# Kernel optimization log

Hardware: AMD Instinct MI355X
Metric: run time of the kernel (lower is better)

## Reference

```python
import jax, jax.numpy as jnp
import numpy as np

N = 100000   # nodes
E = 1600000  # edges
IN_DIM, HID, HEADS, OUT_DIM = 8, 64, 4, 3


def _add_self_loops(src, dst, n):
    loop = jnp.arange(n, dtype=src.dtype)
    return jnp.concatenate([src, loop]), jnp.concatenate([dst, loop])


def gcn_conv(x, src, dst, n, W, b):
    # PyG GCNConv: add self-loops, symmetric normalization deg^-1/2 * deg^-1/2
    s, d = _add_self_loops(src, dst, n)
    deg = jax.ops.segment_sum(jnp.ones(s.shape[0], x.dtype), d, num_segments=n)
    dinv = jnp.where(deg > 0, jax.lax.rsqrt(deg), 0.0)
    norm = dinv[s] * dinv[d]                       # [E']
    h = x @ W                                      # [N, out]
    out = jax.ops.segment_sum(norm[:, None] * h[s], d, num_segments=n)
    return out + b


def gat_conv(x, src, dst, n, W, att_src, att_dst, b):
    # PyG GATConv, concat=True, negative_slope=0.2, self-loops added
    h = (x @ W).reshape(n, HEADS, HID)             # [N, H, C]
    s, d = _add_self_loops(src, dst, n)
    a_src = jnp.sum(h * att_src, axis=-1)          # [N, H]
    a_dst = jnp.sum(h * att_dst, axis=-1)          # [N, H]
    e = jax.nn.leaky_relu(a_src[s] + a_dst[d], negative_slope=0.2)  # [E', H]
    m = jax.lax.stop_gradient(jax.ops.segment_max(e, d, num_segments=n))
    ex = jnp.exp(e - m[d])
    denom = jax.ops.segment_sum(ex, d, num_segments=n)
    alpha = ex / (denom[d] + 1e-16)                # segment softmax over incoming edges
    out = jax.ops.segment_sum(alpha[:, :, None] * h[s], d, num_segments=n)  # [N, H, C]
    return out.reshape(n, HEADS * HID) + b


def setup_inputs() -> dict:
    key = jax.random.key(0)
    ks = jax.random.split(key, 16)
    def glorot(k, shape):
        fan = shape[0] + shape[-1]
        return jax.random.normal(k, shape, jnp.float32) * np.sqrt(2.0 / fan)
    return {
        "x": jax.random.normal(ks[0], (N, IN_DIM), jnp.float32),
        "edge_index": jax.random.randint(ks[1], (2, E), 0, N, jnp.int64 if jax.config.jax_enable_x64 else jnp.int32),
        "w1": glorot(ks[2], (IN_DIM, HID)), "b1": jnp.zeros((HID,), jnp.float32),
        "w2": glorot(ks[3], (HID, HID)),   "b2": jnp.zeros((HID,), jnp.float32),
        "w3": glorot(ks[4], (HID, HID)),   "b3": jnp.zeros((HID,), jnp.float32),
        "wg": glorot(ks[5], (HID, HEADS * HID)), "bg": jnp.zeros((HEADS * HID,), jnp.float32),
        "att_src": glorot(ks[6], (HEADS, HID)),
        "att_dst": glorot(ks[7], (HEADS, HID)),
        "wc1": glorot(ks[8], (HEADS * HID, HID)), "bc1": jnp.zeros((HID,), jnp.float32),
        "wc2": glorot(ks[9], (HID, OUT_DIM)),     "bc2": jnp.zeros((OUT_DIM,), jnp.float32),
    }


def reference(x, edge_index, w1, b1, w2, b2, w3, b3, wg, bg, att_src, att_dst, wc1, bc1, wc2, bc2):
    src, dst = edge_index[0], edge_index[1]
    n = x.shape[0]
    # stacked GCN convs with ReLU; residual when shapes match (layers 2,3)
    h = jax.nn.relu(gcn_conv(x, src, dst, n, w1, b1))
    h = h + jax.nn.relu(gcn_conv(h, src, dst, n, w2, b2))
    h = h + jax.nn.relu(gcn_conv(h, src, dst, n, w3, b3))
    # GAT attention layer (4 heads, concat)
    h_att = gat_conv(h, src, dst, n, wg, att_src, att_dst, bg)  # [N, 256]
    # classifier MLP (dropout is inference no-op)
    z = jax.nn.relu(h_att @ wc1 + bc1)
    logits = z @ wc2 + bc2
    return jax.nn.log_softmax(logits, axis=1)
```

## Files before the change

kernel.cpp:

```cpp
#include <hip/hip_runtime.h>
#include <math.h>


typedef _Float16 half8 __attribute__((ext_vector_type(8)));
typedef _Float16 f16x8 __attribute__((ext_vector_type(8)));
typedef float f32x4 __attribute__((ext_vector_type(4)));
typedef int int4v __attribute__((ext_vector_type(4)));

#define BCAP 210000

__device__ __forceinline__ float leaky02(float v) { return v > 0.f ? v : 0.2f * v; }


template <int CTRL>
__device__ __forceinline__ float dpp_add(float v) {
    int iv = __builtin_bit_cast(int, v);
    int r = __builtin_amdgcn_update_dpp(iv, iv, CTRL, 0xF, 0xF, false);
    return v + __builtin_bit_cast(float, r);
}
template <int OFF>
__device__ __forceinline__ float swz_add(float v) {
    int r = __builtin_amdgcn_ds_swizzle(__builtin_bit_cast(int, v), OFF);
    return v + __builtin_bit_cast(float, r);
}
template <int CTRL>
__device__ __forceinline__ float dpp_max(float v) {
    int iv = __builtin_bit_cast(int, v);
    int r = __builtin_amdgcn_update_dpp(iv, iv, CTRL, 0xF, 0xF, false);
    return fmaxf(v, __builtin_bit_cast(float, r));
}
template <int OFF>
__device__ __forceinline__ float swz_max(float v) {
    int r = __builtin_amdgcn_ds_swizzle(__builtin_bit_cast(int, v), OFF);
    return fmaxf(v, __builtin_bit_cast(float, r));
}
__device__ __forceinline__ float red8(float v) {
    v = dpp_add<0xB1>(v);
    v = dpp_add<0x4E>(v);
    v = swz_add<0x101F>(v);
    return v;
}
__device__ __forceinline__ float red16(float v) {
    v = dpp_add<0xB1>(v);
    v = dpp_add<0x4E>(v);
    v = swz_add<0x101F>(v);
    v = dpp_add<0x128>(v);
    return v;
}
__device__ __forceinline__ float red16max(float v) {
    v = dpp_max<0xB1>(v);
    v = dpp_max<0x4E>(v);
    v = swz_max<0x101F>(v);
    v = dpp_max<0x128>(v);
    return v;
}
__device__ __forceinline__ float red64(float v) {
    v = dpp_add<0xB1>(v);
    v = dpp_add<0x4E>(v);
    v = swz_add<0x101F>(v);
    v = dpp_add<0x128>(v);
    v = swz_add<0x401F>(v);
    v = v + __shfl_xor(v, 32);
    return v;
}
__device__ __forceinline__ float red32max(float v) {
    v = dpp_max<0xB1>(v);
    v = dpp_max<0x4E>(v);
    v = swz_max<0x101F>(v);
    v = dpp_max<0x128>(v);
    v = swz_max<0x401F>(v);
    return v;
}


__global__ __launch_bounds__(256) void bucketize(
        const int* __restrict__ src, const int* __restrict__ dst,
        int E, int range,
        int* __restrict__ bucketCur, int* __restrict__ bSrc, int* __restrict__ bDst) {
    __shared__ unsigned sScan[4][256];
    __shared__ unsigned long long sPair[2048];
    __shared__ int sBase[8];
    __shared__ int sLds[9];
    int tid = threadIdx.x;
    int e0 = blockIdx.x * 2048 + tid * 8;

    int d[8], s[8], rr[8];
    bool ok[8];
    if (e0 + 7 < E) {
        int4v da = *(const int4v*)(dst + e0);
        int4v db = *(const int4v*)(dst + e0 + 4);
        int4v sa = *(const int4v*)(src + e0);
        int4v sb = *(const int4v*)(src + e0 + 4);
#pragma unroll
        for (int j = 0; j < 4; ++j) { d[j] = da[j]; d[j + 4] = db[j]; s[j] = sa[j]; s[j + 4] = sb[j]; ok[j] = true; ok[j + 4] = true; }
    } else {
#pragma unroll
        for (int j = 0; j < 8; ++j) {
            ok[j] = (e0 + j < E);
            d[j] = ok[j] ? dst[e0 + j] : 0;
            s[j] = ok[j] ? src[e0 + j] : 0;
        }
    }
    unsigned hcnt = 0;
#pragma unroll
    for (int j = 0; j < 8; ++j) {
        int r = min(d[j] / range, 7);
        rr[j] = r;
        if (ok[j]) hcnt += 1u << (r * 4);
    }
#pragma unroll
    for (int k = 0; k < 4; ++k)
        sScan[k][tid] = ((hcnt >> (k * 8)) & 0xF) | (((hcnt >> (k * 8 + 4)) & 0xF) << 16);
    __syncthreads();
    for (int off = 1; off < 256; off <<= 1) {
        unsigned v0 = (tid >= off) ? sScan[0][tid - off] : 0;
        unsigned v1 = (tid >= off) ? sScan[1][tid - off] : 0;
        unsigned v2 = (tid >= off) ? sScan[2][tid - off] : 0;
        unsigned v3 = (tid >= off) ? sScan[3][tid - off] : 0;
        __syncthreads();
        sScan[0][tid] += v0; sScan[1][tid] += v1; sScan[2][tid] += v2; sScan[3][tid] += v3;
        __syncthreads();
    }
    if (tid < 8) {
        int k = tid >> 1, sh = (tid & 1) * 16;
        int tot = (sScan[k][255] >> sh) & 0xFFFF;
        sBase[tid] = atomicAdd(&bucketCur[tid], tot);
    }
    if (tid == 0) {
        int run = 0;
#pragma unroll
        for (int r = 0; r < 8; ++r) {
            sLds[r] = run;
            run += (sScan[r >> 1][255] >> ((r & 1) * 16)) & 0xFFFF;
        }
        sLds[8] = run;
    }
    __syncthreads();
    unsigned placed = 0;
#pragma unroll
    for (int j = 0; j < 8; ++j) {
        if (ok[j]) {
            int r = rr[j];
            int k = r >> 1, sh = (r & 1) * 16;
            int incl = (sScan[k][tid] >> sh) & 0xFFFF;
            int mine = (hcnt >> (r * 4)) & 0xF;
            int ex = incl - mine;
            int pc = (placed >> (r * 4)) & 0xF;
            placed += 1u << (r * 4);
            sPair[sLds[r] + ex + pc] =
                ((unsigned long long)(unsigned)d[j] << 32) | (unsigned)s[j];
        }
    }
    __syncthreads();
    int btotal = sLds[8];
    for (int i = tid; i < btotal; i += 256) {
        unsigned long long p = sPair[i];
        int r = 0;
#pragma unroll
        for (int k = 1; k < 8; ++k) r += (i >= sLds[k]);
        size_t g = (size_t)r * BCAP + sBase[r] + (i - sLds[r]);
        bSrc[g] = (int)(unsigned)(p & 0xFFFFFFFFu);
        bDst[g] = (int)(unsigned)(p >> 32);
    }
}

__global__ void count_b(const int* __restrict__ bDst,
                        const int* __restrict__ bucketCur,
                        int* __restrict__ counts) {
    int grp = blockIdx.x & 7;
    int cnt = bucketCur[grp];
    const int* bd = bDst + (size_t)grp * BCAP;
    int nblk = gridDim.x >> 3;
    int c = blockIdx.x >> 3;
    int stride4 = nblk * blockDim.x * 4;
    for (int e = (c * blockDim.x + threadIdx.x) * 4; e < cnt; e += stride4) {
        if (e + 3 < cnt) {
            int4v d4 = *(const int4v*)(bd + e);
#pragma unroll
            for (int j = 0; j < 4; ++j) atomicAdd(&counts[d4[j]], 1);
        } else {
#pragma unroll
            for (int j = 0; j < 4; ++j)
                if (e + j < cnt) atomicAdd(&counts[bd[e + j]], 1);
        }
    }
}

__global__ void scan_pass1(const int* __restrict__ counts, int n, int* __restrict__ blockSums) {
    __shared__ int sh[256];
    int base = blockIdx.x * 2048;
    int tid = threadIdx.x;
    int s = 0;
#pragma unroll
    for (int j = 0; j < 8; ++j) {
        int idx = base + tid * 8 + j;
        if (idx < n) s += counts[idx];
    }
    sh[tid] = s;
    __syncthreads();
    for (int off = 128; off > 0; off >>= 1) {
        if (tid < off) sh[tid] += sh[tid + off];
        __syncthreads();
    }
    if (tid == 0) blockSums[blockIdx.x] = sh[0];
}

__global__ void scan_pass2(const int* __restrict__ blockSums, int nb, int* __restrict__ blockOffs) {
    if (threadIdx.x == 0 && blockIdx.x == 0) {
        int run = 0;
        for (int i = 0; i < nb; ++i) { blockOffs[i] = run; run += blockSums[i]; }
    }
}

__global__ void scan_pass3(const int* __restrict__ counts, int n,
                           const int* __restrict__ blockOffs,
                           const float* __restrict__ x,
                           int* __restrict__ row_ptr, int* __restrict__ cursor,
                           float* __restrict__ dinv, float* __restrict__ rdinv,
                           _Float16* __restrict__ xs,
                           int* __restrict__ shortList, int* __restrict__ longList,
                           int* __restrict__ nodeCnts) {
    __shared__ int sh[256];
    __shared__ int shp[256];
    __shared__ int baseS, baseL;
    int base = blockIdx.x * 2048;
    int tid = threadIdx.x;
    int cnt[8];
    int local = 0;
#pragma unroll
    for (int j = 0; j < 8; ++j) {
        int idx = base + tid * 8 + j;
        cnt[j] = (idx < n) ? counts[idx] : 0;
        local += cnt[j];
    }
    sh[tid] = local;
    __syncthreads();
    for (int off = 1; off < 256; off <<= 1) {
        int v = (tid >= off) ? sh[tid - off] : 0;
        __syncthreads();
        sh[tid] += v;
        __syncthreads();
    }
    int run = blockOffs[blockIdx.x] + sh[tid] - local;
#pragma unroll
    for (int j = 0; j < 8; ++j) {
        int idx = base + tid * 8 + j;
        if (idx < n) {
            row_ptr[idx] = run;
            cursor[idx] = run;
            float dv = rsqrtf((float)(cnt[j] + 1));
            dinv[idx] = dv;
            rdinv[idx] = sqrtf((float)(cnt[j] + 1));
#pragma unroll
            for (int t = 0; t < 8; ++t) xs[idx * 8 + t] = (_Float16)(dv * x[idx * 8 + t]);
            run += cnt[j];
            if (idx == n - 1) row_ptr[n] = run;
        }
    }
    int myS = 0, myL = 0;
#pragma unroll
    for (int j = 0; j < 8; ++j) {
        int idx = base + tid * 8 + j;
        if (idx < n) { if (cnt[j] <= 15) ++myS; else ++myL; }
    }
    shp[tid] = myS | (myL << 16);
    __syncthreads();
    for (int off = 1; off < 256; off <<= 1) {
        int v = (tid >= off) ? shp[tid - off] : 0;
        __syncthreads();
        shp[tid] += v;
        __syncthreads();
    }
    if (tid == 255) {
        baseS = atomicAdd(&nodeCnts[0], shp[255] & 0xFFFF);
        baseL = atomicAdd(&nodeCnts[1], shp[255] >> 16);
    }
    __syncthreads();
    int pS = baseS + (shp[tid] & 0xFFFF) - myS;
    int pL = baseL + (shp[tid] >> 16) - myL;
#pragma unroll
    for (int j = 0; j < 8; ++j) {
        int idx = base + tid * 8 + j;
        if (idx < n) {
            if (cnt[j] <= 15) shortList[pS++] = idx;
            else              longList[pL++] = idx;
        }
    }
}

__global__ void scatter_b(const int* __restrict__ bSrc, const int* __restrict__ bDst,
                          const int* __restrict__ bucketCur,
                          int* __restrict__ cursor, int* __restrict__ col_src) {
    int grp = blockIdx.x & 7;
    int cnt = bucketCur[grp];
    const int* bd = bDst + (size_t)grp * BCAP;
    const int* bs = bSrc + (size_t)grp * BCAP;
    int nblk = gridDim.x >> 3;
    int c = blockIdx.x >> 3;
    int stride4 = nblk * blockDim.x * 4;
    for (int e = (c * blockDim.x + threadIdx.x) * 4; e < cnt; e += stride4) {
        if (e + 3 < cnt) {
            int4v d4 = *(const int4v*)(bd + e);
            int4v s4 = *(const int4v*)(bs + e);
#pragma unroll
            for (int j = 0; j < 4; ++j) {
                int pos = atomicAdd(&cursor[d4[j]], 1);
                col_src[pos] = s4[j];
            }
        } else {
#pragma unroll
            for (int j = 0; j < 4; ++j) {
                if (e + j < cnt) {
                    int pos = atomicAdd(&cursor[bd[e + j]], 1);
                    col_src[pos] = bs[e + j];
                }
            }
        }
    }
}


__global__ void ccomb_kernel(const float* __restrict__ Wg, const float* __restrict__ bg,
                             const float* __restrict__ wc1, const float* __restrict__ bc1,
                             const float* __restrict__ att_src, const float* __restrict__ att_dst,
                             const float* __restrict__ w2, const float* __restrict__ w3,
                             _Float16* __restrict__ CcombP, float* __restrict__ bcomb,
                             float* __restrict__ wse, float* __restrict__ wde,
                             _Float16* __restrict__ W2P, _Float16* __restrict__ W3P) {
    int bid = blockIdx.x;
    int j = threadIdx.x;
    if (bid < 256) {
        int i = bid;
        float s = 0.f;
        for (int c = 0; c < 64; ++c)
            s += Wg[(i & 63) * 256 + (i >> 6) * 64 + c] * wc1[((i >> 6) * 64 + c) * 64 + j];
        _Float16 hi = (_Float16)s;
        _Float16 lo = (_Float16)(s - (float)hi);
        int kt = i >> 5, l = (((i >> 3) & 3) << 4) | (j & 15), e = i & 7, ct = j >> 4;
        CcombP[(ct * 8 + kt) * 512 + l * 8 + e] = hi;
        CcombP[(32 + ct * 8 + kt) * 512 + l * 8 + e] = lo;
    } else if (bid == 256) {
        float s = bc1[j];
        for (int i = 0; i < 256; ++i) s += bg[i] * wc1[i * 64 + j];
        bcomb[j] = s;
#pragma unroll
        for (int h = 0; h < 4; ++h) {
            float ss = 0.f, sd = 0.f;
            for (int c = 0; c < 64; ++c) {
                float w = Wg[j * 256 + h * 64 + c];
                ss += w * att_src[h * 64 + c];
                sd += w * att_dst[h * 64 + c];
            }
            wse[j * 4 + h] = ss;
            wde[j * 4 + h] = sd;
        }
    } else {
        int i = (bid < 321) ? (bid - 257) : (bid - 321);
        const float* W = (bid < 321) ? w2 : w3;
        _Float16* WP = (bid < 321) ? W2P : W3P;
        float s = W[i * 64 + j];
        _Float16 hi = (_Float16)s;
        _Float16 lo = (_Float16)(s - (float)hi);
        int kt = i >> 5, l = (((i >> 3) & 3) << 4) | (j & 15), e = i & 7, ct = j >> 4;
        WP[(ct * 2 + kt) * 512 + l * 8 + e] = hi;
        WP[(8 + ct * 2 + kt) * 512 + l * 8 + e] = lo;
    }
}


__global__ void gcn_layer1(const half8* __restrict__ xs8,
                           const float* __restrict__ W1, const float* __restrict__ b1,
                           const int* __restrict__ row_ptr, const int* __restrict__ col_src,
                           const float* __restrict__ dinv, int n,
                           _Float16* __restrict__ hs1) {
    int tid = threadIdx.x, lane = tid & 63, wid = tid >> 6;
    int node = blockIdx.x * 4 + wid;
    if (node >= n) return;
    int beg = row_ptr[node], end = row_ptr[node + 1];
    int deg = end - beg;
    float acc[8] = {0.f, 0.f, 0.f, 0.f, 0.f, 0.f, 0.f, 0.f};
    for (int base = 0; base < deg; base += 64) {
        int cs = col_src[min(beg + base + lane, end - 1)];
        half8 v = xs8[cs];
        if (base + lane < deg) {
#pragma unroll
            for (int c = 0; c < 8; ++c) acc[c] += (float)v[c];
        }
    }
#pragma unroll
    for (int c = 0; c < 8; ++c) acc[c] = red64(acc[c]);
    half8 sv = xs8[node];
    float di = dinv[node];
    float agg[8];
#pragma unroll
    for (int c = 0; c < 8; ++c) agg[c] = (acc[c] + (float)sv[c]) * di;
    float sum = b1[lane];
#pragma unroll
    for (int k = 0; k < 8; ++k) sum = fmaf(agg[k], W1[k * 64 + lane], sum);
    hs1[node * 64 + lane] = (_Float16)(di * fmaxf(sum, 0.f));
}


__global__ void gcn_agg(const _Float16* __restrict__ hs_in,
                        const int* __restrict__ row_ptr, const int* __restrict__ col_src,
                        const float* __restrict__ dinv, int n,
                        _Float16* __restrict__ aggout) {
    int tid = threadIdx.x, lane = tid & 63, wid = tid >> 6;
    int node = blockIdx.x * 4 + wid;
    if (node >= n) return;
    int t = lane >> 3, g = lane & 7;
    const half8* hs8 = (const half8*)hs_in;
    int beg = row_ptr[node], end = row_ptr[node + 1];
    int deg = end - beg;
    half8 sv = hs8[node * 8 + t];
    float ac[8];
#pragma unroll
    for (int c = 0; c < 8; ++c) ac[c] = (g == 0) ? (float)sv[c] : 0.f;
    for (int base = 0; base < deg; base += 64) {
        int cs = col_src[min(beg + base + lane, end - 1)];
        int lim = min(deg - base, 64);
        auto bodyF = [&](int eo8) {
            int s = __shfl(cs, eo8 + g);
            half8 v = hs8[s * 8 + t];
#pragma unroll
            for (int c = 0; c < 8; ++c) ac[c] += (float)v[c];
        };
        auto bodyG = [&](int eo8) {
            int eo = eo8 + g;
            int s = __shfl(cs, eo);
            half8 v = hs8[s * 8 + t];
            if (eo < lim) {
#pragma unroll
                for (int c = 0; c < 8; ++c) ac[c] += (float)v[c];
            }
        };
        int eo8 = 0;
        for (; eo8 + 16 <= lim; eo8 += 16) { bodyF(eo8); bodyF(eo8 + 8); }
        if (eo8 < lim) {
            bodyG(eo8);
            eo8 += 8;
            if (eo8 < lim) bodyG(eo8);
        }
    }
    float di = dinv[node];
#pragma unroll
    for (int c = 0; c < 8; ++c) ac[c] = red8(ac[c]) * di;
    if (g == 0) {
        half8 hv;
#pragma unroll
        for (int c = 0; c < 8; ++c) hv[c] = (_Float16)ac[c];
        *(half8*)(aggout + (size_t)node * 64 + t * 8) = hv;
    }
}


template <bool LAST>
__global__ __launch_bounds__(256) void gcn_mfma(
        const _Float16* __restrict__ agg,
        const _Float16* __restrict__ WP,
        const float* __restrict__ b,
        const _Float16* __restrict__ hs_in,
        const float* __restrict__ dinv, const float* __restrict__ rdinv,
        const float* __restrict__ wse, const float* __restrict__ wde,
        int n, _Float16* __restrict__ hout,
        float4* __restrict__ a_src4, float4* __restrict__ a_dst4) {
    __shared__ float partS[4][16][4];
    __shared__ float partD[4][16][4];
    int tid = threadIdx.x;
    int lane = tid & 63;
    int w = __builtin_amdgcn_readfirstlane(tid >> 6);
    int c16 = lane & 15, hi = lane >> 4;

    f16x8 bh[2], blo[2];
#pragma unroll
    for (int kt = 0; kt < 2; ++kt) {
        bh[kt]  = *(const f16x8*)(WP + (size_t)(w * 2 + kt) * 512 + lane * 8);
        blo[kt] = *(const f16x8*)(WP + (size_t)(8 + w * 2 + kt) * 512 + lane * 8);
    }
    int col = w * 16 + c16;
    float bl = b[col];
    float4 wev, wdv;
    if (LAST) {
        wev = ((const float4*)wse)[col];
        wdv = ((const float4*)wde)[col];
    }

    int ntiles = (n + 15) >> 4;
    for (int tile = blockIdx.x; tile < ntiles; tile += gridDim.x) {
        int rowb = tile * 16;
        int arow = min(rowb + c16, n - 1);
        const _Float16* ap = agg + (size_t)arow * 64 + hi * 8;
        f16x8 a0 = *(const f16x8*)(ap);
        f16x8 a1 = *(const f16x8*)(ap + 32);
        f32x4 acc = {0.f, 0.f, 0.f, 0.f};
        acc = __builtin_amdgcn_mfma_f32_16x16x32_f16(a0, bh[0],  acc, 0, 0, 0);
        acc = __builtin_amdgcn_mfma_f32_16x16x32_f16(a0, blo[0], acc, 0, 0, 0);
        acc = __builtin_amdgcn_mfma_f32_16x16x32_f16(a1, bh[1],  acc, 0, 0, 0);
        acc = __builtin_amdgcn_mfma_f32_16x16x32_f16(a1, blo[1], acc, 0, 0, 0);
#pragma unroll
        for (int r = 0; r < 4; ++r) {
            int noder = rowb + hi * 4 + r;
            bool ok = noder < n;
            int ni = min(noder, n - 1);
            float hp = rdinv[ni] * (float)hs_in[(size_t)ni * 64 + col];
            float z = fmaxf(acc[r] + bl, 0.f);
            float hv = hp + z;
            if (!LAST) {
                if (ok) hout[(size_t)ni * 64 + col] = (_Float16)(dinv[ni] * hv);
            } else {
                if (ok) hout[(size_t)ni * 64 + col] = (_Float16)hv;
                float s0 = red16(hv * wev.x), s1 = red16(hv * wev.y);
                float s2 = red16(hv * wev.z), s3 = red16(hv * wev.w);
                float d0 = red16(hv * wdv.x), d1 = red16(hv * wdv.y);
                float d2 = red16(hv * wdv.z), d3 = red16(hv * wdv.w);
                if (c16 == 0) {
                    *(float4*)&partS[w][hi * 4 + r][0] = make_float4(s0, s1, s2, s3);
                    *(float4*)&partD[w][hi * 4 + r][0] = make_float4(d0, d1, d2, d3);
                }
            }
        }
        if (LAST) {
            __syncthreads();
            if (tid < 16) {
                int node = rowb + tid;
                if (node < n) {
                    float4 s = make_float4(
                        partS[0][tid][0] + partS[1][tid][0] + partS[2][tid][0] + partS[3][tid][0],
                        partS[0][tid][1] + partS[1][tid][1] + partS[2][tid][1] + partS[3][tid][1],
                        partS[0][tid][2] + partS[1][tid][2] + partS[2][tid][2] + partS[3][tid][2],
                        partS[0][tid][3] + partS[1][tid][3] + partS[2][tid][3] + partS[3][tid][3]);
                    float4 d = make_float4(
                        partD[0][tid][0] + partD[1][tid][0] + partD[2][tid][0] + partD[3][tid][0],
                        partD[0][tid][1] + partD[1][tid][1] + partD[2][tid][1] + partD[3][tid][1],
                        partD[0][tid][2] + partD[1][tid][2] + partD[2][tid][2] + partD[3][tid][2],
                        partD[0][tid][3] + partD[1][tid][3] + partD[2][tid][3] + partD[3][tid][3]);
                    a_src4[node] = s;
                    a_dst4[node] = d;
                }
            }
            __syncthreads();
        }
    }
}


__global__ __launch_bounds__(256, 4) void gat_agg_short(
        const _Float16* __restrict__ h3,
        const float4* __restrict__ a_src4, const float4* __restrict__ a_dst4,
        const int* __restrict__ row_ptr, const int* __restrict__ col_src,
        const int* __restrict__ shortList, const int* __restrict__ nodeCnts,
        _Float16* __restrict__ aggout) {
    __shared__ _Float16 HsAll[4][32 * 72];
    __shared__ _Float16 wATAll[4][16 * 40];
    int tid = threadIdx.x, lane = tid & 63, wid = tid >> 6;
    int nshort = nodeCnts[0];
    int i0 = (blockIdx.x * 4 + wid) * 2;
    if (i0 >= nshort) return;
    int nodeA = shortList[i0];
    int nodeB = (i0 + 1 < nshort) ? shortList[i0 + 1] : nodeA;
    _Float16* Hs = HsAll[wid];
    _Float16* wAT = wATAll[wid];

    {
        int zm = lane >> 2;
        int zc = ((zm < 8) ? 16 : 0) + (lane & 3) * 4;
#pragma unroll
        for (int j = 0; j < 4; ++j) wAT[zm * 40 + zc + j] = (_Float16)0.f;
    }

    int q = lane >> 4, m16 = lane & 15;
    int c0 = (lane & 7) * 8;
    int sl16 = lane & 15;
    int myNode = (lane < 16) ? nodeA : ((lane < 32) ? nodeB : nodeA);
    int begL = row_ptr[myNode], endL = row_ptr[myNode + 1];
    int nslL = endL - begL + 1;
    float4 adv = a_dst4[myNode];
    int eidx = max(min(begL + sl16 - 1, endL - 1), 0);
    int cs = (sl16 == 0) ? myNode : col_src[eidx];
    float4 as = a_src4[cs];
    float vm = (sl16 < nslL && lane < 32) ? 1.f : 0.f;
    float l0 = leaky02(as.x + adv.x);
    float l1 = leaky02(as.y + adv.y);
    float l2 = leaky02(as.z + adv.z);
    float l3 = leaky02(as.w + adv.w);
    float m0 = red16max(vm > 0.f ? l0 : -1e30f);
    float m1 = red16max(vm > 0.f ? l1 : -1e30f);
    float m2 = red16max(vm > 0.f ? l2 : -1e30f);
    float m3 = red16max(vm > 0.f ? l3 : -1e30f);
    float w0 = vm * __expf(fminf(l0 - m0, 10.f));
    float w1 = vm * __expf(fminf(l1 - m1, 10.f));
    float w2 = vm * __expf(fminf(l2 - m2, 10.f));
    float w3 = vm * __expf(fminf(l3 - m3, 10.f));
    if (lane < 32) {
        int rb = (lane < 16) ? 0 : 8;
        int k = lane;
        _Float16 h0 = (_Float16)w0, h1 = (_Float16)w1;
        _Float16 h2 = (_Float16)w2, h3v = (_Float16)w3;
        wAT[(rb + 0) * 40 + k] = h0;
        wAT[(rb + 1) * 40 + k] = h1;
        wAT[(rb + 2) * 40 + k] = h2;
        wAT[(rb + 3) * 40 + k] = h3v;
        wAT[(rb + 4) * 40 + k] = (_Float16)(w0 - (float)h0);
        wAT[(rb + 5) * 40 + k] = (_Float16)(w1 - (float)h1);
        wAT[(rb + 6) * 40 + k] = (_Float16)(w2 - (float)h2);
        wAT[(rb + 7) * 40 + k] = (_Float16)(w3 - (float)h3v);
    }
#pragma unroll
    for (int i = 0; i < 4; ++i) {
        int r = i * 8 + (lane >> 3);
        int s = __shfl(cs, r);
        half8 hv = *(const half8*)(h3 + (size_t)s * 64 + c0);
        *(half8*)(Hs + r * 72 + (c0 ^ (i << 4))) = hv;
    }
    __asm__ volatile("s_waitcnt lgkmcnt(0)" ::: "memory");
    f16x8 A = *(const f16x8*)(wAT + m16 * 40 + q * 8);
    int swz = q << 4;
    const _Float16* Bb0 = Hs + (size_t)q * 8 * 72 + ((0 * 16 + m16) ^ swz);
    const _Float16* Bb1 = Hs + (size_t)q * 8 * 72 + ((1 * 16 + m16) ^ swz);
    const _Float16* Bb2 = Hs + (size_t)q * 8 * 72 + ((2 * 16 + m16) ^ swz);
    const _Float16* Bb3 = Hs + (size_t)q * 8 * 72 + ((3 * 16 + m16) ^ swz);
    f16x8 B0, B1, B2, B3;
#pragma unroll
    for (int e = 0; e < 8; ++e) {
        B0[e] = Bb0[e * 72];
        B1[e] = Bb1[e * 72];
        B2[e] = Bb2[e * 72];
        B3[e] = Bb3[e * 72];
    }
    f16x8 ONES;
#pragma unroll
    for (int e = 0; e < 8; ++e) ONES[e] = (_Float16)1.f;
    f32x4 acc0 = {0.f,0.f,0.f,0.f}, acc1 = {0.f,0.f,0.f,0.f};
    f32x4 acc2 = {0.f,0.f,0.f,0.f}, acc3 = {0.f,0.f,0.f,0.f};
    f32x4 accD = {0.f,0.f,0.f,0.f};
    acc0 = __builtin_amdgcn_mfma_f32_16x16x32_f16(A, B0, acc0, 0, 0, 0);
    acc1 = __builtin_amdgcn_mfma_f32_16x16x32_f16(A, B1, acc1, 0, 0, 0);
    acc2 = __builtin_amdgcn_mfma_f32_16x16x32_f16(A, B2, acc2, 0, 0, 0);
    acc3 = __builtin_amdgcn_mfma_f32_16x16x32_f16(A, B3, acc3, 0, 0, 0);
    accD = __builtin_amdgcn_mfma_f32_16x16x32_f16(A, ONES, accD, 0, 0, 0);

    float tot[4][4], rdv[4];
#pragma unroll
    for (int r = 0; r < 4; ++r) {
        tot[0][r] = acc0[r] + __shfl_xor(acc0[r], 16);
        tot[1][r] = acc1[r] + __shfl_xor(acc1[r], 16);
        tot[2][r] = acc2[r] + __shfl_xor(acc2[r], 16);
        tot[3][r] = acc3[r] + __shfl_xor(acc3[r], 16);
        float d = accD[r] + __shfl_xor(accD[r], 16);
        rdv[r] = 1.f / (d + 1e-16f);
    }
    int outNode = -1;
    if (lane < 16) outNode = nodeA;
    else if (lane >= 32 && lane < 48 && nodeB != nodeA) outNode = nodeB;
    if (outNode >= 0) {
        size_t ob = (size_t)outNode * 256 + (lane & 15);
#pragma unroll
        for (int r = 0; r < 4; ++r) {
#pragma unroll
            for (int ct = 0; ct < 4; ++ct)
                aggout[ob + r * 64 + ct * 16] = (_Float16)(tot[ct][r] * rdv[r]);
        }
    }
}


__global__ __launch_bounds__(256, 4) void gat_agg_long(
        const _Float16* __restrict__ h3,
        const float4* __restrict__ a_src4, const float4* __restrict__ a_dst4,
        const int* __restrict__ row_ptr, const int* __restrict__ col_src,
        const int* __restrict__ longList, const int* __restrict__ nodeCnts,
        _Float16* __restrict__ aggout) {
    __shared__ _Float16 HsAll[4][32 * 72];
    __shared__ _Float16 wATAll[4][16 * 40];
    int tid = threadIdx.x, lane = tid & 63, wid = tid >> 6;
    int nlong = nodeCnts[1];
    int li = blockIdx.x * 4 + wid;
    if (li >= nlong) return;
    int node = longList[li];
    _Float16* Hs = HsAll[wid];
    _Float16* wAT = wATAll[wid];

    int q = lane >> 4, m16 = lane & 15;
    float4 ad = a_dst4[node];
    int beg = row_ptr[node], end = row_ptr[node + 1];
    int deg = end - beg;
    int nslots = deg + 1;
    int c0 = (lane & 7) * 8;

    int swz = q << 4;
    const _Float16* Bb0 = Hs + (size_t)q * 8 * 72 + ((0 * 16 + m16) ^ swz);
    const _Float16* Bb1 = Hs + (size_t)q * 8 * 72 + ((1 * 16 + m16) ^ swz);
    const _Float16* Bb2 = Hs + (size_t)q * 8 * 72 + ((2 * 16 + m16) ^ swz);
    const _Float16* Bb3 = Hs + (size_t)q * 8 * 72 + ((3 * 16 + m16) ^ swz);
    const f16x8* Ab = (const f16x8*)(wAT + m16 * 40 + q * 8);
    f16x8 ONES;
#pragma unroll
    for (int e = 0; e < 8; ++e) ONES[e] = (_Float16)1.f;

    f32x4 acc0 = {0.f,0.f,0.f,0.f}, acc1 = {0.f,0.f,0.f,0.f};
    f32x4 acc2 = {0.f,0.f,0.f,0.f}, acc3 = {0.f,0.f,0.f,0.f};
    f32x4 accD = {0.f,0.f,0.f,0.f};
    float m0 = 0.f, m1 = 0.f, m2 = 0.f, m3 = 0.f;

    for (int base = 0; base < nslots; base += 32) {
        int sl = base + (lane & 31);
        int eidx = max(min(beg + sl - 1, end - 1), 0);
        int cs = (sl == 0) ? node : col_src[eidx];
        float4 as = a_src4[cs];
        float vm = (sl < nslots && lane < 32) ? 1.f : 0.f;
        float l0 = leaky02(as.x + ad.x);
        float l1 = leaky02(as.y + ad.y);
        float l2 = leaky02(as.z + ad.z);
        float l3 = leaky02(as.w + ad.w);
        if (base == 0) {
            m0 = red32max(vm > 0.f ? l0 : -1e30f);
            m1 = red32max(vm > 0.f ? l1 : -1e30f);
            m2 = red32max(vm > 0.f ? l2 : -1e30f);
            m3 = red32max(vm > 0.f ? l3 : -1e30f);
        }
        float w0 = vm * __expf(fminf(l0 - m0, 10.f));
        float w1 = vm * __expf(fminf(l1 - m1, 10.f));
        float w2 = vm * __expf(fminf(l2 - m2, 10.f));
        float w3 = vm * __expf(fminf(l3 - m3, 10.f));
        if (lane < 32) {
            int s32 = lane & 31;
            _Float16 h0 = (_Float16)w0, h1 = (_Float16)w1;
            _Float16 h2 = (_Float16)w2, h3v = (_Float16)w3;
            wAT[0 * 40 + s32] = h0;
            wAT[1 * 40 + s32] = h1;
            wAT[2 * 40 + s32] = h2;
            wAT[3 * 40 + s32] = h3v;
            wAT[4 * 40 + s32] = (_Float16)(w0 - (float)h0);
            wAT[5 * 40 + s32] = (_Float16)(w1 - (float)h1);
            wAT[6 * 40 + s32] = (_Float16)(w2 - (float)h2);
            wAT[7 * 40 + s32] = (_Float16)(w3 - (float)h3v);
        }
#pragma unroll
        for (int i = 0; i < 4; ++i) {
            int r = i * 8 + (lane >> 3);
            int s = __shfl(cs, r);
            half8 hv = *(const half8*)(h3 + (size_t)s * 64 + c0);
            *(half8*)(Hs + r * 72 + (c0 ^ (i << 4))) = hv;
        }
        __asm__ volatile("s_waitcnt lgkmcnt(0)" ::: "memory");
        f16x8 A = *Ab;
        f16x8 B0, B1, B2, B3;
#pragma unroll
        for (int e = 0; e < 8; ++e) {
            B0[e] = Bb0[e * 72];
            B1[e] = Bb1[e * 72];
            B2[e] = Bb2[e * 72];
            B3[e] = Bb3[e * 72];
        }
        acc0 = __builtin_amdgcn_mfma_f32_16x16x32_f16(A, B0, acc0, 0, 0, 0);
        acc1 = __builtin_amdgcn_mfma_f32_16x16x32_f16(A, B1, acc1, 0, 0, 0);
        acc2 = __builtin_amdgcn_mfma_f32_16x16x32_f16(A, B2, acc2, 0, 0, 0);
        acc3 = __builtin_amdgcn_mfma_f32_16x16x32_f16(A, B3, acc3, 0, 0, 0);
        accD = __builtin_amdgcn_mfma_f32_16x16x32_f16(A, ONES, accD, 0, 0, 0);
        __asm__ volatile("s_waitcnt lgkmcnt(0)" ::: "memory");
    }

    float tot[4][4], rdv[4];
#pragma unroll
    for (int r = 0; r < 4; ++r) {
        tot[0][r] = acc0[r] + __shfl_xor(acc0[r], 16);
        tot[1][r] = acc1[r] + __shfl_xor(acc1[r], 16);
        tot[2][r] = acc2[r] + __shfl_xor(acc2[r], 16);
        tot[3][r] = acc3[r] + __shfl_xor(acc3[r], 16);
        float d = accD[r] + __shfl_xor(accD[r], 16);
        rdv[r] = 1.f / (d + 1e-16f);
    }
    if (lane < 16) {
        size_t ob = (size_t)node * 256 + lane;
#pragma unroll
        for (int r = 0; r < 4; ++r) {
#pragma unroll
            for (int ct = 0; ct < 4; ++ct)
                aggout[ob + r * 64 + ct * 16] = (_Float16)(tot[ct][r] * rdv[r]);
        }
    }
}


__global__ __launch_bounds__(256) void mlp_mfma(
        const _Float16* __restrict__ agg,
        const _Float16* __restrict__ CP,
        const float* __restrict__ bcomb,
        const float* __restrict__ wc2, const float* __restrict__ bc2,
        int n, float* __restrict__ out) {
    __shared__ float part[4][16][3];
    int tid = threadIdx.x;
    int lane = tid & 63;
    int w = __builtin_amdgcn_readfirstlane(tid >> 6);
    int c16 = lane & 15, hi = lane >> 4;

    f16x8 bh[8], blo[8];
#pragma unroll
    for (int kt = 0; kt < 8; ++kt) {
        bh[kt]  = *(const f16x8*)(CP + (size_t)(w * 8 + kt) * 512 + lane * 8);
        blo[kt] = *(const f16x8*)(CP + (size_t)(32 + w * 8 + kt) * 512 + lane * 8);
    }
    int col = w * 16 + c16;
    float bc  = bcomb[col];
    float w20 = wc2[col * 3 + 0], w21 = wc2[col * 3 + 1], w22 = wc2[col * 3 + 2];
    float bb0 = bc2[0], bb1 = bc2[1], bb2 = bc2[2];

    int ntiles = (n + 15) >> 4;
    for (int tile = blockIdx.x; tile < ntiles; tile += gridDim.x) {
        int rowb = tile * 16;
        int row = min(rowb + c16, n - 1);
        const _Float16* ap = agg + (size_t)row * 256 + hi * 8;
        f16x8 a[8];
#pragma unroll
        for (int kt = 0; kt < 8; ++kt) a[kt] = *(const f16x8*)(ap + kt * 32);
        f32x4 acc = {0.f, 0.f, 0.f, 0.f};
#pragma unroll
        for (int kt = 0; kt < 8; ++kt) {
            acc = __builtin_amdgcn_mfma_f32_16x16x32_f16(a[kt], bh[kt],  acc, 0, 0, 0);
            acc = __builtin_amdgcn_mfma_f32_16x16x32_f16(a[kt], blo[kt], acc, 0, 0, 0);
        }
        float pr[4][3];
#pragma unroll
        for (int r = 0; r < 4; ++r) {
            float z = fmaxf(acc[r] + bc, 0.f);
            pr[r][0] = red16(z * w20);
            pr[r][1] = red16(z * w21);
            pr[r][2] = red16(z * w22);
        }
        if (c16 == 0) {
#pragma unroll
            for (int r = 0; r < 4; ++r) {
                part[w][hi * 4 + r][0] = pr[r][0];
                part[w][hi * 4 + r][1] = pr[r][1];
                part[w][hi * 4 + r][2] = pr[r][2];
            }
        }
        __syncthreads();
        if (tid < 16) {
            int node = rowb + tid;
            if (node < n) {
                float e0 = part[0][tid][0] + part[1][tid][0] + part[2][tid][0] + part[3][tid][0] + bb0;
                float e1 = part[0][tid][1] + part[1][tid][1] + part[2][tid][1] + part[3][tid][1] + bb1;
                float e2 = part[0][tid][2] + part[1][tid][2] + part[2][tid][2] + part[3][tid][2] + bb2;
                float mx = fmaxf(e0, fmaxf(e1, e2));
                float lse = mx + logf(expf(e0 - mx) + expf(e1 - mx) + expf(e2 - mx));
                out[(size_t)node * 3 + 0] = e0 - lse;
                out[(size_t)node * 3 + 1] = e1 - lse;
                out[(size_t)node * 3 + 2] = e2 - lse;
            }
        }
        __syncthreads();
    }
}


extern "C" void kernel_launch(void* const* d_in, const int* in_sizes, int n_in,
                              void* d_out, int out_size, void* d_ws, size_t ws_size,
                              hipStream_t stream) {
    const float* x       = (const float*)d_in[0];
    const int*   ei      = (const int*)d_in[1];
    const float* w1      = (const float*)d_in[2];
    const float* b1      = (const float*)d_in[3];
    const float* w2      = (const float*)d_in[4];
    const float* b2      = (const float*)d_in[5];
    const float* w3      = (const float*)d_in[6];
    const float* b3      = (const float*)d_in[7];
    const float* wg      = (const float*)d_in[8];
    const float* bg      = (const float*)d_in[9];
    const float* att_s   = (const float*)d_in[10];
    const float* att_d   = (const float*)d_in[11];
    const float* wc1     = (const float*)d_in[12];
    const float* bc1     = (const float*)d_in[13];
    const float* wc2     = (const float*)d_in[14];
    const float* bc2     = (const float*)d_in[15];
    float* out = (float*)d_out;

    const int N = in_sizes[0] / 8;
    const int E = in_sizes[1] / 2;
    const int* srcv = ei;
    const int* dstv = ei + E;

    char* ws = (char*)d_ws;
    size_t off = 0;
    auto alloc = [&](size_t bytes) -> char* {
        char* p = ws + off;
        off += (bytes + 255) & ~(size_t)255;
        return p;
    };
    int*      counts    = (int*)alloc((size_t)N * 4);
    int*      row_ptr   = (int*)alloc((size_t)(N + 1) * 4);
    int*      cursor    = (int*)alloc((size_t)N * 4);
    int*      col_src   = (int*)alloc((size_t)E * 4);
    int*      blockSums = (int*)alloc(4096 * 4);
    int*      blockOffs = (int*)alloc(4096 * 4);
    float*    dinv      = (float*)alloc((size_t)N * 4);
    float*    rdinv     = (float*)alloc((size_t)N * 4);
    _Float16* xs        = (_Float16*)alloc((size_t)N * 8 * 2);
    float*    a_src     = (float*)alloc((size_t)N * 16);
    float*    a_dst     = (float*)alloc((size_t)N * 16);
    float*    wse       = (float*)alloc(256 * 4);
    float*    wde       = (float*)alloc(256 * 4);
    _Float16* CcombP    = (_Float16*)alloc(64 * 1024);
    float*    bcomb     = (float*)alloc(64 * 4);
    _Float16* W2P       = (_Float16*)alloc(16 * 1024);
    _Float16* W3P       = (_Float16*)alloc(16 * 1024);
    int*      shortList = (int*)alloc((size_t)N * 4);
    int*      longList  = (int*)alloc((size_t)N * 4);
    int*      nodeCnts  = (int*)alloc(256);
    int*      bucketCur = (int*)alloc(256);
    _Float16* bufA      = (_Float16*)alloc((size_t)N * 64 * 2);
    _Float16* bufB      = (_Float16*)alloc((size_t)N * 64 * 2);
    _Float16* aggbuf    = (_Float16*)alloc((size_t)N * 256 * 2);
    _Float16* hs1 = bufA;
    _Float16* hs2 = bufB;
    _Float16* h3  = bufA;
    _Float16* aggA = aggbuf;
    int* bSrc = (int*)aggbuf;
    int* bDst = bSrc + (size_t)8 * BCAP;
    (void)ws_size; (void)n_in; (void)out_size;

    hipMemsetAsync(counts, 0, (size_t)N * 4, stream);
    hipMemsetAsync(nodeCnts, 0, 8, stream);
    hipMemsetAsync(bucketCur, 0, 32, stream);

    const int TPB = 256;
    int range = (N + 7) / 8;

    int gridBk = (E + 2047) / 2048;
    bucketize<<<gridBk, TPB, 0, stream>>>(srcv, dstv, E, range, bucketCur, bSrc, bDst);
    count_b<<<2048, TPB, 0, stream>>>(bDst, bucketCur, counts);

    int NB = (N + 2047) / 2048;
    scan_pass1<<<NB, TPB, 0, stream>>>(counts, N, blockSums);
    scan_pass2<<<1, 64, 0, stream>>>(blockSums, NB, blockOffs);
    scan_pass3<<<NB, TPB, 0, stream>>>(counts, N, blockOffs, x,
                                       row_ptr, cursor, dinv, rdinv, xs,
                                       shortList, longList, nodeCnts);
    scatter_b<<<2048, TPB, 0, stream>>>(bSrc, bDst, bucketCur, cursor, col_src);

    ccomb_kernel<<<385, 64, 0, stream>>>(wg, bg, wc1, bc1, att_s, att_d, w2, w3,
                                         CcombP, bcomb, wse, wde, W2P, W3P);

    int gridN = (N + 3) / 4;
    gcn_layer1<<<gridN, TPB, 0, stream>>>((const half8*)xs, w1, b1, row_ptr, col_src,
                                          dinv, N, hs1);

    gcn_agg<<<gridN, TPB, 0, stream>>>(hs1, row_ptr, col_src, dinv, N, aggA);
    gcn_mfma<false><<<2048, TPB, 0, stream>>>(aggA, W2P, b2, hs1, dinv, rdinv,
                                              nullptr, nullptr, N, hs2,
                                              nullptr, nullptr);
    gcn_agg<<<gridN, TPB, 0, stream>>>(hs2, row_ptr, col_src, dinv, N, aggA);
    gcn_mfma<true><<<2048, TPB, 0, stream>>>(aggA, W3P, b3, hs2, dinv, rdinv,
                                             wse, wde, N, h3,
                                             (float4*)a_src, (float4*)a_dst);

    int gridS = ((N + 1) / 2 + 3) / 4;
    gat_agg_short<<<gridS, TPB, 0, stream>>>(h3, (const float4*)a_src,
                                             (const float4*)a_dst, row_ptr, col_src,
                                             shortList, nodeCnts, aggbuf);
    gat_agg_long<<<gridN, TPB, 0, stream>>>(h3, (const float4*)a_src,
                                            (const float4*)a_dst, row_ptr, col_src,
                                            longList, nodeCnts, aggbuf);
    mlp_mfma<<<2048, TPB, 0, stream>>>(aggbuf, CcombP, bcomb, wc2, bc2, N, out);
}
```

Baseline: 530.0 us.

## Assign edge buckets to blocks by XCC id with atomic work-stealing tickets

Measured after the change: 871.9 us. 1.65x slower.

```diff
diff --git a/kernel.cpp b/kernel.cpp
--- a/kernel.cpp
+++ b/kernel.cpp
@@ -10,6 +10,12 @@
 #define BCAP 210000
 
 __device__ __forceinline__ float leaky02(float v) { return v > 0.f ? v : 0.2f * v; }
+
+__device__ __forceinline__ int xcc_id() {
+    int x;
+    asm volatile("s_getreg_b32 %0, hwreg(20)" : "=s"(x));
+    return x & 7;
+}
 
 
 template <int CTRL>
@@ -166,22 +172,31 @@
 
 __global__ void count_b(const int* __restrict__ bDst,
                         const int* __restrict__ bucketCur,
-                        int* __restrict__ counts) {
-    int grp = blockIdx.x & 7;
-    int cnt = bucketCur[grp];
-    const int* bd = bDst + (size_t)grp * BCAP;
-    int nblk = gridDim.x >> 3;
-    int c = blockIdx.x >> 3;
-    int stride4 = nblk * blockDim.x * 4;
-    for (int e = (c * blockDim.x + threadIdx.x) * 4; e < cnt; e += stride4) {
-        if (e + 3 < cnt) {
-            int4v d4 = *(const int4v*)(bd + e);
-#pragma unroll
-            for (int j = 0; j < 4; ++j) atomicAdd(&counts[d4[j]], 1);
-        } else {
-#pragma unroll
-            for (int j = 0; j < 4; ++j)
-                if (e + j < cnt) atomicAdd(&counts[bd[e + j]], 1);
+                        int* __restrict__ counts, int* __restrict__ tickets) {
+    __shared__ int sT;
+    int tid = threadIdx.x;
+    int myg = xcc_id();
+    for (int pass = 0; pass < 8; ++pass) {
+        int g = (myg + pass) & 7;
+        int cnt = bucketCur[g];
+        const int* bd = bDst + (size_t)g * BCAP;
+        for (;;) {
+            if (tid == 0) sT = atomicAdd(&tickets[g], 1);
+            __syncthreads();
+            int chunk = sT;
+            __syncthreads();
+            int e0 = chunk * 1024;
+            if (e0 >= cnt) break;
+            int e = e0 + tid * 4;
+            if (e + 3 < cnt) {
+                int4v d4 = *(const int4v*)(bd + e);
+#pragma unroll
+                for (int j = 0; j < 4; ++j) atomicAdd(&counts[d4[j]], 1);
+            } else {
+#pragma unroll
+                for (int j = 0; j < 4; ++j)
+                    if (e + j < cnt) atomicAdd(&counts[bd[e + j]], 1);
+            }
         }
     }
 }
@@ -290,29 +305,39 @@
 
 __global__ void scatter_b(const int* __restrict__ bSrc, const int* __restrict__ bDst,
                           const int* __restrict__ bucketCur,
-                          int* __restrict__ cursor, int* __restrict__ col_src) {
-    int grp = blockIdx.x & 7;
-    int cnt = bucketCur[grp];
-    const int* bd = bDst + (size_t)grp * BCAP;
-    const int* bs = bSrc + (size_t)grp * BCAP;
-    int nblk = gridDim.x >> 3;
-    int c = blockIdx.x >> 3;
-    int stride4 = nblk * blockDim.x * 4;
-    for (int e = (c * blockDim.x + threadIdx.x) * 4; e < cnt; e += stride4) {
-        if (e + 3 < cnt) {
-            int4v d4 = *(const int4v*)(bd + e);
-            int4v s4 = *(const int4v*)(bs + e);
-#pragma unroll
-            for (int j = 0; j < 4; ++j) {
-                int pos = atomicAdd(&cursor[d4[j]], 1);
-                col_src[pos] = s4[j];
-            }
-        } else {
-#pragma unroll
-            for (int j = 0; j < 4; ++j) {
-                if (e + j < cnt) {
-                    int pos = atomicAdd(&cursor[bd[e + j]], 1);
-                    col_src[pos] = bs[e + j];
+                          int* __restrict__ cursor, int* __restrict__ col_src,
+                          int* __restrict__ tickets) {
+    __shared__ int sT;
+    int tid = threadIdx.x;
+    int myg = xcc_id();
+    for (int pass = 0; pass < 8; ++pass) {
+        int g = (myg + pass) & 7;
+        int cnt = bucketCur[g];
+        const int* bd = bDst + (size_t)g * BCAP;
+        const int* bs = bSrc + (size_t)g * BCAP;
+        for (;;) {
+            if (tid == 0) sT = atomicAdd(&tickets[g], 1);
+            __syncthreads();
+            int chunk = sT;
+            __syncthreads();
+            int e0 = chunk * 1024;
+            if (e0 >= cnt) break;
+            int e = e0 + tid * 4;
+            if (e + 3 < cnt) {
+                int4v d4 = *(const int4v*)(bd + e);
+                int4v s4 = *(const int4v*)(bs + e);
+#pragma unroll
+                for (int j = 0; j < 4; ++j) {
+                    int pos = atomicAdd(&cursor[d4[j]], 1);
+                    col_src[pos] = s4[j];
+                }
+            } else {
+#pragma unroll
+                for (int j = 0; j < 4; ++j) {
+                    if (e + j < cnt) {
+                        int pos = atomicAdd(&cursor[bd[e + j]], 1);
+                        col_src[pos] = bs[e + j];
+                    }
                 }
             }
         }
@@ -908,6 +933,7 @@
     int*      longList  = (int*)alloc((size_t)N * 4);
     int*      nodeCnts  = (int*)alloc(256);
     int*      bucketCur = (int*)alloc(256);
+    int*      tickets   = (int*)alloc(256);
     _Float16* bufA      = (_Float16*)alloc((size_t)N * 64 * 2);
     _Float16* bufB      = (_Float16*)alloc((size_t)N * 64 * 2);
     _Float16* aggbuf    = (_Float16*)alloc((size_t)N * 256 * 2);
@@ -922,13 +948,14 @@
     hipMemsetAsync(counts, 0, (size_t)N * 4, stream);
     hipMemsetAsync(nodeCnts, 0, 8, stream);
     hipMemsetAsync(bucketCur, 0, 32, stream);
+    hipMemsetAsync(tickets, 0, 64, stream);
 
     const int TPB = 256;
     int range = (N + 7) / 8;
 
     int gridBk = (E + 2047) / 2048;
     bucketize<<<gridBk, TPB, 0, stream>>>(srcv, dstv, E, range, bucketCur, bSrc, bDst);
-    count_b<<<2048, TPB, 0, stream>>>(bDst, bucketCur, counts);
+    count_b<<<2048, TPB, 0, stream>>>(bDst, bucketCur, counts, tickets);
 
     int NB = (N + 2047) / 2048;
     scan_pass1<<<NB, TPB, 0, stream>>>(counts, N, blockSums);
@@ -936,7 +963,8 @@
     scan_pass3<<<NB, TPB, 0, stream>>>(counts, N, blockOffs, x,
                                        row_ptr, cursor, dinv, rdinv, xs,
                                        shortList, longList, nodeCnts);
-    scatter_b<<<2048, TPB, 0, stream>>>(bSrc, bDst, bucketCur, cursor, col_src);
+    scatter_b<<<2048, TPB, 0, stream>>>(bSrc, bDst, bucketCur, cursor, col_src,
+                                        tickets + 8);
 
     ccomb_kernel<<<385, 64, 0, stream>>>(wg, bg, wc1, bc1, att_s, att_d, w2, w3,
                                          CcombP, bcomb, wse, wde, W2P, W3P);
```
